# Optimization experiments

Measured on AMD Instinct MI355X. Metric: run time of the kernel, lower is better.

Reference implementation:

```python
import jax, jax.numpy as jnp
import numpy as np

EPS = 1e-5

def _bn(h, gamma, beta):
    # training-mode batch norm over dim 0 (biased variance, as torch)
    mu = h.mean(axis=0)
    var = ((h - mu) ** 2).mean(axis=0)
    return (h - mu) * jax.lax.rsqrt(var + EPS) * gamma + beta

def _mlp(h, W1, b1, g1, be1, W2, b2):
    # PyG MLP, num_layers=2: Linear -> BatchNorm -> ReLU -> Linear (dropout=0)
    h = h @ W1 + b1
    h = jax.nn.relu(_bn(h, g1, be1))
    return h @ W2 + b2

def setup_inputs() -> dict:
    key = jax.random.key(0)
    ks = jax.random.split(key, 12)
    N, E = 50000, 800000
    node_dim, edge_dim, hidden = 64, 64, 128
    d_in1 = node_dim + edge_dim   # 128
    d_in2 = node_dim + hidden     # 192
    def lin(k, fi, fo):
        s = 1.0 / np.sqrt(fi)
        return jax.random.uniform(k, (fi, fo), jnp.float32, -s, s)
    inp = {
        "x": jax.random.normal(ks[0], (N, node_dim), jnp.float32),
        "edge_index": jax.random.randint(ks[1], (2, E), 0, N, jnp.int32),
        "edge_attr": jax.random.normal(ks[2], (E, edge_dim), jnp.float32),
        "u": jax.random.normal(ks[3], (1, 16), jnp.float32),
        "batch": jnp.zeros((N,), jnp.int32),
        # node_mlp_1 params
        "W1a": lin(ks[4], d_in1, hidden), "b1a": jnp.zeros((hidden,), jnp.float32),
        "g1a": jnp.ones((hidden,), jnp.float32), "be1a": jnp.zeros((hidden,), jnp.float32),
        "W2a": lin(ks[5], hidden, hidden), "b2a": jnp.zeros((hidden,), jnp.float32),
        # node_mlp_2 params
        "W1b": lin(ks[6], d_in2, hidden), "b1b": jnp.zeros((hidden,), jnp.float32),
        "g1b": jnp.ones((hidden,), jnp.float32), "be1b": jnp.zeros((hidden,), jnp.float32),
        "W2b": lin(ks[7], hidden, node_dim), "b2b": jnp.zeros((node_dim,), jnp.float32),
    }
    return inp

def reference(x, edge_index, edge_attr, u, batch,
              W1a, b1a, g1a, be1a, W2a, b2a,
              W1b, b1b, g1b, be1b, W2b, b2b):
    row, col = edge_index[0], edge_index[1]
    # gather source nodes, concat edge features  -> [E, node_dim+edge_dim]
    out = jnp.concatenate([x[row], edge_attr], axis=1)
    out = _mlp(out, W1a, b1a, g1a, be1a, W2a, b2a)          # [E, hidden]
    out = jax.ops.segment_sum(out, col, num_segments=x.shape[0])  # scatter_add -> [N, hidden]
    out = jnp.concatenate([x, out], axis=1)                  # [N, node_dim+hidden]
    return _mlp(out, W1b, b1b, g1b, be1b, W2b, b2b)          # [N, node_dim]
```

## Files before the change

kernel.cpp:

```cpp
#include <hip/hip_runtime.h>
#include <hip/hip_fp16.h>


typedef _Float16 half8  __attribute__((ext_vector_type(8)));
typedef _Float16 half4h __attribute__((ext_vector_type(4)));
typedef float    floatx4 __attribute__((ext_vector_type(4)));

#define MFMA16(a, b, c) __builtin_amdgcn_mfma_f32_16x16x32_f16(a, b, c, 0, 0, 0)

#define LDS_BARRIER() do { \
    asm volatile("s_waitcnt lgkmcnt(0)" ::: "memory"); \
    __builtin_amdgcn_s_barrier(); \
} while (0)

__device__ __forceinline__ float col_reduce16(float v) {
    v += __shfl_xor(v, 16, 64);
    v += __shfl_xor(v, 32, 64);
    return v;
}

__global__ void k_prep(const float* __restrict__ w1a, const float* __restrict__ w2a,
                       const float* __restrict__ w1b, const float* __restrict__ w2b,
                       _Float16* __restrict__ w1at, _Float16* __restrict__ w2at,
                       _Float16* __restrict__ w1bt, _Float16* __restrict__ w2bt) {
    int i = blockIdx.x * 256 + threadIdx.x;
    if (i < 16384) {
        int n = i >> 7, k = i & 127;
        w1at[n * 128 + k] = (_Float16)w1a[k * 128 + n];
    } else if (i < 32768) {
        int j = i - 16384; int n = j >> 7, k = j & 127;
        w2at[n * 128 + k] = (_Float16)w2a[k * 128 + n];
    } else if (i < 57344) {
        int j = i - 32768; int n = j / 192, k = j - n * 192;
        w1bt[n * 192 + k] = (_Float16)w1b[k * 128 + n];
    } else if (i < 65536) {
        int j = i - 57344; int n = j >> 7, k = j & 127;
        w2bt[n * 128 + k] = (_Float16)w2b[k * 64 + n];
    }
}

__global__ __launch_bounds__(512, 4) void k_edge_stats(
    const float* __restrict__ x, const int* __restrict__ rowi,
    const float* __restrict__ ea, const _Float16* __restrict__ w1t,
    float* __restrict__ gsum, float* __restrict__ gsq, int nTiles) {
    __shared__ _Float16 sW[128][136];
    __shared__ _Float16 sIn[128][136];
    const int tid = threadIdx.x, lane = tid & 63, wv = tid >> 6;
    const int lm = lane & 15, q = lane >> 4, koff = q * 8;
    const int G = gridDim.x;
    const int e = tid >> 2, part = tid & 3;

    {
        int n = tid >> 2, seg = (tid & 3) * 32;
        const half8* src = (const half8*)(w1t + n * 128 + seg);
        half8* dst = (half8*)&sW[n][seg];
        dst[0] = src[0]; dst[1] = src[1]; dst[2] = src[2]; dst[3] = src[3];
    }
    float sAcc[8], ssAcc[8];
#pragma unroll
    for (int i = 0; i < 8; i++) { sAcc[i] = 0.f; ssAcc[i] = 0.f; }

    int t = blockIdx.x;
    floatx4 pv[8];
    {
        long ge = (long)t * 128 + e;
        const float* src = (part < 2) ? x + (long)rowi[ge] * 64 + part * 32
                                      : ea + ge * 64 + (part - 2) * 32;
#pragma unroll
        for (int i = 0; i < 8; i++) pv[i] = ((const floatx4*)src)[i];
    }
    for (; t < nTiles; t += G) {
        {
            _Float16* dst = &sIn[e][part * 32];
#pragma unroll
            for (int i = 0; i < 8; i++) {
                half4h h = {(_Float16)pv[i][0], (_Float16)pv[i][1],
                            (_Float16)pv[i][2], (_Float16)pv[i][3]};
                *(half4h*)(dst + i * 4) = h;
            }
        }
        LDS_BARRIER();
        int tn = t + G;
        if (tn < nTiles) {
            long ge = (long)tn * 128 + e;
            const float* src = (part < 2) ? x + (long)rowi[ge] * 64 + part * 32
                                          : ea + ge * 64 + (part - 2) * 32;
#pragma unroll
            for (int i = 0; i < 8; i++) pv[i] = ((const floatx4*)src)[i];
        }
        half8 a[4];
#pragma unroll
        for (int kb = 0; kb < 4; kb++)
            a[kb] = *(const half8*)&sIn[wv * 16 + lm][kb * 32 + koff];
#pragma unroll
        for (int nt = 0; nt < 8; nt++) {
            floatx4 acc = {0.f, 0.f, 0.f, 0.f};
            const int c = nt * 16 + lm;
#pragma unroll
            for (int kb = 0; kb < 4; kb++) {
                half8 b = *(const half8*)&sW[c][kb * 32 + koff];
                acc = MFMA16(a[kb], b, acc);
            }
            sAcc[nt]  += acc[0] + acc[1] + acc[2] + acc[3];
            ssAcc[nt] += acc[0]*acc[0] + acc[1]*acc[1] + acc[2]*acc[2] + acc[3]*acc[3];
        }
        LDS_BARRIER();
    }
#pragma unroll
    for (int nt = 0; nt < 8; nt++) {
        float s  = col_reduce16(sAcc[nt]);
        float ss = col_reduce16(ssAcc[nt]);
        if (q == 0) {
            int c = nt * 16 + lm;
            int slot = (blockIdx.x * 8 + wv) & 15;
            unsafeAtomicAdd(&gsum[slot * 128 + c], s);
            unsafeAtomicAdd(&gsq[slot * 128 + c], ss);
        }
    }
}

__global__ void k_finalize(const float* __restrict__ sums, const float* __restrict__ sqs,
                           const float* __restrict__ gamma, const float* __restrict__ beta,
                           float* __restrict__ scale, float* __restrict__ shift, float count) {
    int i = threadIdx.x;
    float s = 0.f, ssq = 0.f;
    for (int j = 0; j < 16; j++) { s += sums[j * 128 + i]; ssq += sqs[j * 128 + i]; }
    float mu = s / count;
    float var = ssq / count - mu * mu;
    float sc = gamma[i] * rsqrtf(var + 1e-5f);
    scale[i] = sc;
    shift[i] = beta[i] - mu * sc;
}

__global__ __launch_bounds__(512, 2) void k_edge_mlp(
    const float* __restrict__ x, const int* __restrict__ rowi, const int* __restrict__ coli,
    const float* __restrict__ ea, const _Float16* __restrict__ w1t, const _Float16* __restrict__ w2t,
    const float* __restrict__ scale, const float* __restrict__ shift, const float* __restrict__ b2a,
    __half* __restrict__ agg, int nTiles) {
    __shared__ _Float16 sW1[128][136];
    __shared__ _Float16 sW2[128][136];
    __shared__ _Float16 sIn[2][128][136];
    __shared__ float sScale[128], sShift[128], sB2[128];
    __shared__ int sCol[2][128];
    const int tid = threadIdx.x, lane = tid & 63, wv = tid >> 6;
    const int lm = lane & 15, q = lane >> 4, koff = q * 8;
    const int G = gridDim.x;
    const int e = tid >> 2, part = tid & 3;

    {
        int n = tid >> 2, seg = (tid & 3) * 32;
        const half8* s1 = (const half8*)(w1t + n * 128 + seg);
        half8* d1 = (half8*)&sW1[n][seg];
        d1[0] = s1[0]; d1[1] = s1[1]; d1[2] = s1[2]; d1[3] = s1[3];
        const half8* s2 = (const half8*)(w2t + n * 128 + seg);
        half8* d2 = (half8*)&sW2[n][seg];
        d2[0] = s2[0]; d2[1] = s2[1]; d2[2] = s2[2]; d2[3] = s2[3];
    }
    if (tid < 128) { sScale[tid] = scale[tid]; sShift[tid] = shift[tid]; sB2[tid] = b2a[tid]; }

    int t = blockIdx.x;
    {
        long ge = (long)t * 128 + e;
        const float* src = (part < 2) ? x + (long)rowi[ge] * 64 + part * 32
                                      : ea + ge * 64 + (part - 2) * 32;
        _Float16* dst = &sIn[0][e][part * 32];
#pragma unroll
        for (int i = 0; i < 8; i++) {
            floatx4 v = ((const floatx4*)src)[i];
            half4h h = {(_Float16)v[0], (_Float16)v[1], (_Float16)v[2], (_Float16)v[3]};
            *(half4h*)(dst + i * 4) = h;
        }
        if (tid < 128) sCol[0][tid] = coli[(long)t * 128 + tid];
    }
    __syncthreads();
    int p = 0;
    for (; t < nTiles; t += G) {
        half8 a[4];
#pragma unroll
        for (int kb = 0; kb < 4; kb++)
            a[kb] = *(const half8*)&sIn[p][wv * 16 + lm][kb * 32 + koff];
        int myCol[4];
#pragma unroll
        for (int r = 0; r < 4; r++) myCol[r] = sCol[p][wv * 16 + q * 4 + r];

        int tn = t + G; bool hasNext = tn < nTiles;
        floatx4 pv[8]; int pcol = 0;
        if (hasNext) {
            long ge = (long)tn * 128 + e;
            const float* src = (part < 2) ? x + (long)rowi[ge] * 64 + part * 32
                                          : ea + ge * 64 + (part - 2) * 32;
#pragma unroll
            for (int i = 0; i < 8; i++) pv[i] = ((const floatx4*)src)[i];
            if (tid < 128) pcol = coli[(long)tn * 128 + tid];
        }
        floatx4 acc1[8];
#pragma unroll
        for (int nt = 0; nt < 8; nt++) {
            floatx4 acc = {0.f, 0.f, 0.f, 0.f};
            const int c = nt * 16 + lm;
#pragma unroll
            for (int kb = 0; kb < 4; kb++) {
                half8 b = *(const half8*)&sW1[c][kb * 32 + koff];
                acc = MFMA16(a[kb], b, acc);
            }
            acc1[nt] = acc;
        }
        LDS_BARRIER();

        _Float16(*sT)[136] = sIn[p];
#pragma unroll
        for (int nt = 0; nt < 8; nt++) {
            const int c = nt * 16 + lm;
            float sc = sScale[c], sh = sShift[c];
            half4h h;
#pragma unroll
            for (int r = 0; r < 4; r++)
                h[r] = (_Float16)fmaxf(acc1[nt][r] * sc + sh, 0.f);
            *(half4h*)&sT[c][wv * 16 + q * 4] = h;
        }
        half8 a2[4];
#pragma unroll
        for (int kb = 0; kb < 4; kb++) {
#pragma unroll
            for (int j = 0; j < 8; j++)
                a2[kb][j] = sT[kb * 32 + koff + j][wv * 16 + lm];
        }
#pragma unroll
        for (int nt = 0; nt < 8; nt++) {
            floatx4 acc = {0.f, 0.f, 0.f, 0.f};
            const int c = nt * 16 + lm;
#pragma unroll
            for (int kb = 0; kb < 4; kb++) {
                half8 b = *(const half8*)&sW2[c][kb * 32 + koff];
                acc = MFMA16(a2[kb], b, acc);
            }
            acc1[nt] = acc;
        }
        if (hasNext) {
            _Float16* dst = &sIn[p ^ 1][e][part * 32];
#pragma unroll
            for (int i = 0; i < 8; i++) {
                half4h h = {(_Float16)pv[i][0], (_Float16)pv[i][1],
                            (_Float16)pv[i][2], (_Float16)pv[i][3]};
                *(half4h*)(dst + i * 4) = h;
            }
            if (tid < 128) sCol[p ^ 1][tid] = pcol;
        }
#pragma unroll
        for (int nt = 0; nt < 8; nt++) {
            const int c = nt * 16 + lm;
            const int c0 = c & ~1;
            float bb = sB2[c];
            float v0 = acc1[nt][0] + bb, v1 = acc1[nt][1] + bb;
            float v2 = acc1[nt][2] + bb, v3 = acc1[nt][3] + bb;
            float p0 = __shfl_xor(v0, 1, 64), p1 = __shfl_xor(v1, 1, 64);
            float p2 = __shfl_xor(v2, 1, 64), p3 = __shfl_xor(v3, 1, 64);
            if ((lane & 1) == 0) {
                unsafeAtomicAdd((__half2*)&agg[(size_t)myCol[0] * 128 + c0], __floats2half2_rn(v0, p0));
                unsafeAtomicAdd((__half2*)&agg[(size_t)myCol[1] * 128 + c0], __floats2half2_rn(v1, p1));
            } else {
                unsafeAtomicAdd((__half2*)&agg[(size_t)myCol[2] * 128 + c0], __floats2half2_rn(p2, v2));
                unsafeAtomicAdd((__half2*)&agg[(size_t)myCol[3] * 128 + c0], __floats2half2_rn(p3, v3));
            }
        }
        LDS_BARRIER();
        p ^= 1;
    }
}

__global__ __launch_bounds__(512, 2) void k_node_a(
    const float* __restrict__ x, const __half* __restrict__ agg,
    const _Float16* __restrict__ w1bt, float* __restrict__ h3,
    float* __restrict__ gsum, float* __restrict__ gsq, int N) {
    __shared__ _Float16 sIn[128][200];
    __shared__ _Float16 sW[128][200];
    __shared__ float sSum[128], sSq[128];
    const int tid = threadIdx.x, lane = tid & 63, wv = tid >> 6;
    const long e0 = (long)blockIdx.x * 128;

    {
        int n = tid >> 2, seg = (tid & 3) * 48;
        const half8* src = (const half8*)(w1bt + n * 192 + seg);
        half8* dst = (half8*)&sW[n][seg];
        dst[0] = src[0]; dst[1] = src[1]; dst[2] = src[2];
        dst[3] = src[3]; dst[4] = src[4]; dst[5] = src[5];
    }
    if (tid < 128) { sSum[tid] = 0.f; sSq[tid] = 0.f; }
    {
        int m = tid >> 2, seg = tid & 3;
        long gm = e0 + m;
        bool valid = gm < N;
        const float* srcx = x + gm * 64 + seg * 16;
        _Float16* dstx = &sIn[m][seg * 16];
#pragma unroll
        for (int i = 0; i < 4; i++) {
            floatx4 v = {0.f, 0.f, 0.f, 0.f};
            if (valid) v = ((const floatx4*)srcx)[i];
            half4h h = {(_Float16)v[0], (_Float16)v[1], (_Float16)v[2], (_Float16)v[3]};
            *(half4h*)(dstx + i * 4) = h;
        }
        const _Float16* srca = (const _Float16*)agg + gm * 128 + seg * 32;
        _Float16* dsta = &sIn[m][64 + seg * 32];
#pragma unroll
        for (int i = 0; i < 4; i++) {
            half8 v = {0, 0, 0, 0, 0, 0, 0, 0};
            if (valid) v = ((const half8*)srca)[i];
            *(half8*)(dsta + i * 8) = v;
        }
    }
    __syncthreads();

    const int lm = lane & 15, q = lane >> 4, koff = q * 8;
    half8 a[6];
#pragma unroll
    for (int kb = 0; kb < 6; kb++)
        a[kb] = *(const half8*)&sIn[wv * 16 + lm][kb * 32 + koff];
#pragma unroll
    for (int nt = 0; nt < 8; nt++) {
        floatx4 acc = {0.f, 0.f, 0.f, 0.f};
        const int c = nt * 16 + lm;
#pragma unroll
        for (int kb = 0; kb < 6; kb++) {
            half8 b = *(const half8*)&sW[c][kb * 32 + koff];
            acc = MFMA16(a[kb], b, acc);
        }
        float s  = acc[0] + acc[1] + acc[2] + acc[3];
        float ss = acc[0]*acc[0] + acc[1]*acc[1] + acc[2]*acc[2] + acc[3]*acc[3];
        s = col_reduce16(s); ss = col_reduce16(ss);
        if (q == 0) { atomicAdd(&sSum[c], s); atomicAdd(&sSq[c], ss); }
#pragma unroll
        for (int r = 0; r < 4; r++) {
            int m2 = wv * 16 + q * 4 + r;
            long gm2 = e0 + m2;
            if (gm2 < N) h3[gm2 * 128 + c] = acc[r];
        }
    }
    __syncthreads();
    if (tid < 128) {
        int slot = blockIdx.x & 15;
        unsafeAtomicAdd(&gsum[slot * 128 + tid], sSum[tid]);
        unsafeAtomicAdd(&gsq[slot * 128 + tid], sSq[tid]);
    }
}

__global__ __launch_bounds__(512, 2) void k_node_b(
    const float* __restrict__ h3, const _Float16* __restrict__ w2bt,
    const float* __restrict__ scale, const float* __restrict__ shift,
    const float* __restrict__ b2b, float* __restrict__ out, int N) {
    __shared__ _Float16 sH[128][136];
    __shared__ _Float16 sW[64][136];
    const int tid = threadIdx.x, lane = tid & 63, wv = tid >> 6;
    const long e0 = (long)blockIdx.x * 128;

    {
        int n = tid >> 3, seg = (tid & 7) * 16;
        const half8* src = (const half8*)(w2bt + n * 128 + seg);
        half8* dst = (half8*)&sW[n][seg];
        dst[0] = src[0]; dst[1] = src[1];
    }
    {
        int m = tid >> 2, seg = (tid & 3) * 32;
        long gm = e0 + m;
        bool valid = gm < N;
        const float* src = h3 + gm * 128 + seg;
        _Float16* dst = &sH[m][seg];
#pragma unroll
        for (int i = 0; i < 8; i++) {
            floatx4 v = {0.f, 0.f, 0.f, 0.f};
            if (valid) v = ((const floatx4*)src)[i];
            floatx4 sc = ((const floatx4*)(scale + seg))[i];
            floatx4 sh = ((const floatx4*)(shift + seg))[i];
            half4h h;
#pragma unroll
            for (int j = 0; j < 4; j++)
                h[j] = (_Float16)fmaxf(v[j] * sc[j] + sh[j], 0.f);
            *(half4h*)(dst + i * 4) = h;
        }
    }
    __syncthreads();

    const int lm = lane & 15, q = lane >> 4, koff = q * 8;
    half8 a[4];
#pragma unroll
    for (int kb = 0; kb < 4; kb++)
        a[kb] = *(const half8*)&sH[wv * 16 + lm][kb * 32 + koff];
#pragma unroll
    for (int nt = 0; nt < 4; nt++) {
        floatx4 acc = {0.f, 0.f, 0.f, 0.f};
        const int c = nt * 16 + lm;
#pragma unroll
        for (int kb = 0; kb < 4; kb++) {
            half8 b = *(const half8*)&sW[c][kb * 32 + koff];
            acc = MFMA16(a[kb], b, acc);
        }
        float bb = b2b[c];
#pragma unroll
        for (int r = 0; r < 4; r++) {
            int m2 = wv * 16 + q * 4 + r;
            long gm2 = e0 + m2;
            if (gm2 < N) out[gm2 * 64 + c] = acc[r] + bb;
        }
    }
}

extern "C" void kernel_launch(void* const* d_in, const int* in_sizes, int n_in,
                              void* d_out, int out_size, void* d_ws, size_t ws_size,
                              hipStream_t stream) {
    const float* x    = (const float*)d_in[0];
    const int*   eidx = (const int*)d_in[1];
    const float* ea   = (const float*)d_in[2];
    const float* W1a  = (const float*)d_in[5];
    const float* g1a  = (const float*)d_in[7];
    const float* be1a = (const float*)d_in[8];
    const float* W2a  = (const float*)d_in[9];
    const float* b2a  = (const float*)d_in[10];
    const float* W1b  = (const float*)d_in[11];
    const float* g1b  = (const float*)d_in[13];
    const float* be1b = (const float*)d_in[14];
    const float* W2b  = (const float*)d_in[15];
    const float* b2b  = (const float*)d_in[16];
    const int N = in_sizes[0] / 64;
    const int E = in_sizes[2] / 64;
    const int* rowi = eidx;
    const int* coli = eidx + E;

    float* ws   = (float*)d_ws;
    __half* agg = (__half*)ws;
    float* h3   = ws + (size_t)N * 64;
    float* st   = h3 + (size_t)N * 128;
    float* sumE = st,        * sqE = st + 2048;
    float* sumN = st + 4096, * sqN = st + 6144;
    float* scE  = st + 8192, * shE = st + 8320;
    float* scN  = st + 8448, * shN = st + 8576;
    _Float16* wh   = (_Float16*)(st + 8704);
    _Float16* w1at = wh;
    _Float16* w2at = wh + 16384;
    _Float16* w1bt = wh + 32768;
    _Float16* w2bt = wh + 57344;

    hipMemsetAsync(agg, 0, (size_t)N * 128 * sizeof(__half), stream);
    hipMemsetAsync(st, 0, 8192 * sizeof(float), stream);
    k_prep<<<256, 256, 0, stream>>>(W1a, W2a, W1b, W2b, w1at, w2at, w1bt, w2bt);

    int nTilesE = E / 128;
    int nbl = (N + 127) / 128;
    k_edge_stats<<<500, 512, 0, stream>>>(x, rowi, ea, w1at, sumE, sqE, nTilesE);
    k_finalize<<<1, 128, 0, stream>>>(sumE, sqE, g1a, be1a, scE, shE, (float)E);
    k_edge_mlp<<<250, 512, 0, stream>>>(x, rowi, coli, ea, w1at, w2at, scE, shE, b2a, agg, nTilesE);
    k_node_a<<<nbl, 512, 0, stream>>>(x, agg, w1bt, h3, sumN, sqN, N);
    k_finalize<<<1, 128, 0, stream>>>(sumN, sqN, g1b, be1b, scN, shN, (float)N);
    k_node_b<<<nbl, 512, 0, stream>>>(h3, w2bt, scN, shN, b2b, (float*)d_out, N);
}
```

Measured before the change: 723.0 us.

## Sort edges by destination and segment-reduce within tiles before atomic adds

Adds a counting sort of edges by destination node (histogram, single-block scan, atomic scatter) that builds permuted row, edge-id and column arrays. The edge MLP kernel then reads edges in destination order and performs a segmented reduction across the 16-row MFMA tile using shuffles, so only one atomic add per run of equal destinations is issued. This is meant to cut the half2 atomic traffic into the aggregation buffer. In exchange it adds three preprocessing kernels, a serial-ish 1024-thread scan, and random (non-coalesced) reads of edge_attr via edge ids.

```diff
diff --git a/kernel.cpp b/kernel.cpp
--- a/kernel.cpp
+++ b/kernel.cpp
@@ -39,6 +39,49 @@
     }
 }
 
+__global__ void k_hist(const int* __restrict__ coli, int* __restrict__ cnt, int E) {
+    int i = blockIdx.x * 512 + threadIdx.x;
+    if (i < E) atomicAdd(&cnt[coli[i]], 1);
+}
+
+__global__ __launch_bounds__(1024) void k_scan(const int* __restrict__ cnt,
+                                               int* __restrict__ cur, int N) {
+    __shared__ int sp[1024];
+    int t = threadIdx.x;
+    int chunk = (N + 1023) >> 10;
+    int base = t * chunk;
+    int s = 0;
+    for (int j = 0; j < chunk; j++) {
+        int idx = base + j;
+        if (idx < N) s += cnt[idx];
+    }
+    sp[t] = s; __syncthreads();
+    for (int off = 1; off < 1024; off <<= 1) {
+        int v = (t >= off) ? sp[t - off] : 0;
+        __syncthreads();
+        sp[t] += v;
+        __syncthreads();
+    }
+    int run = sp[t] - s;
+    for (int j = 0; j < chunk; j++) {
+        int idx = base + j;
+        if (idx < N) { cur[idx] = run; run += cnt[idx]; }
+    }
+}
+
+__global__ void k_scatter(const int* __restrict__ rowi, const int* __restrict__ coli,
+                          int* __restrict__ cur, int* __restrict__ rowp,
+                          int* __restrict__ eidp, int* __restrict__ colp, int E) {
+    int i = blockIdx.x * 512 + threadIdx.x;
+    if (i < E) {
+        int c = coli[i];
+        int p = atomicAdd(&cur[c], 1);
+        rowp[p] = rowi[i];
+        eidp[p] = i;
+        colp[p] = c;
+    }
+}
+
 __global__ __launch_bounds__(512, 4) void k_edge_stats(
     const float* __restrict__ x, const int* __restrict__ rowi,
     const float* __restrict__ ea, const _Float16* __restrict__ w1t,
@@ -133,7 +176,8 @@
 }
 
 __global__ __launch_bounds__(512, 2) void k_edge_mlp(
-    const float* __restrict__ x, const int* __restrict__ rowi, const int* __restrict__ coli,
+    const float* __restrict__ x, const int* __restrict__ rowp, const int* __restrict__ eidp,
+    const int* __restrict__ colp,
     const float* __restrict__ ea, const _Float16* __restrict__ w1t, const _Float16* __restrict__ w2t,
     const float* __restrict__ scale, const float* __restrict__ shift, const float* __restrict__ b2a,
     __half* __restrict__ agg, int nTiles) {
@@ -161,8 +205,9 @@
     int t = blockIdx.x;
     {
         long ge = (long)t * 128 + e;
-        const float* src = (part < 2) ? x + (long)rowi[ge] * 64 + part * 32
-                                      : ea + ge * 64 + (part - 2) * 32;
+        int idx = (part < 2) ? rowp[ge] : eidp[ge];
+        const float* src = (part < 2) ? x + (long)idx * 64 + part * 32
+                                      : ea + (long)idx * 64 + (part - 2) * 32;
         _Float16* dst = &sIn[0][e][part * 32];
 #pragma unroll
         for (int i = 0; i < 8; i++) {
@@ -170,7 +215,7 @@
             half4h h = {(_Float16)v[0], (_Float16)v[1], (_Float16)v[2], (_Float16)v[3]};
             *(half4h*)(dst + i * 4) = h;
         }
-        if (tid < 128) sCol[0][tid] = coli[(long)t * 128 + tid];
+        if (tid < 128) sCol[0][tid] = colp[(long)t * 128 + tid];
     }
     __syncthreads();
     int p = 0;
@@ -180,18 +225,35 @@
         for (int kb = 0; kb < 4; kb++)
             a[kb] = *(const half8*)&sIn[p][wv * 16 + lm][kb * 32 + koff];
         int myCol[4];
-#pragma unroll
-        for (int r = 0; r < 4; r++) myCol[r] = sCol[p][wv * 16 + q * 4 + r];
+        const int m0 = wv * 16 + q * 4;
+#pragma unroll
+        for (int r = 0; r < 4; r++) myCol[r] = sCol[p][m0 + r];
+        int cp = sCol[p][(q > 0) ? m0 - 1 : m0];
+        int cn = sCol[p][(q < 3) ? m0 + 4 : m0 + 3];
+        const bool h0 = (q == 0) || (myCol[0] != cp);
+        const bool h1 = myCol[1] != myCol[0];
+        const bool h2 = myCol[2] != myCol[1];
+        const bool h3 = myCol[3] != myCol[2];
+        const bool t0 = h1, t1 = h2, t2 = h3;
+        const bool t3 = (q == 3) || (myCol[3] != cn);
+        const bool c0m = !h0, c1m = c0m && !h1, c2m = c1m && !h2, c3m = c2m && !h3;
+        const int F0 = (h0 | h1 | h2 | h3) ? 1 : 0;
+        int Fp1 = __shfl(F0, (lane - 16) & 63, 64);
+        const bool add1 = (q >= 1) && !F0;
+        const int F1 = (F0 || ((q >= 1) && Fp1)) ? 1 : 0;
+        const bool add2 = (q >= 2) && !F1;
+        const bool useC = (q >= 1) && !h0;
 
         int tn = t + G; bool hasNext = tn < nTiles;
         floatx4 pv[8]; int pcol = 0;
         if (hasNext) {
             long ge = (long)tn * 128 + e;
-            const float* src = (part < 2) ? x + (long)rowi[ge] * 64 + part * 32
-                                          : ea + ge * 64 + (part - 2) * 32;
+            int idx = (part < 2) ? rowp[ge] : eidp[ge];
+            const float* src = (part < 2) ? x + (long)idx * 64 + part * 32
+                                          : ea + (long)idx * 64 + (part - 2) * 32;
 #pragma unroll
             for (int i = 0; i < 8; i++) pv[i] = ((const floatx4*)src)[i];
-            if (tid < 128) pcol = coli[(long)tn * 128 + tid];
+            if (tid < 128) pcol = colp[(long)tn * 128 + tid];
         }
         floatx4 acc1[8];
 #pragma unroll
@@ -253,14 +315,29 @@
             float bb = sB2[c];
             float v0 = acc1[nt][0] + bb, v1 = acc1[nt][1] + bb;
             float v2 = acc1[nt][2] + bb, v3 = acc1[nt][3] + bb;
-            float p0 = __shfl_xor(v0, 1, 64), p1 = __shfl_xor(v1, 1, 64);
-            float p2 = __shfl_xor(v2, 1, 64), p3 = __shfl_xor(v3, 1, 64);
+            float s0 = v0;
+            float s1 = h1 ? v1 : (s0 + v1);
+            float s2 = h2 ? v2 : (s1 + v2);
+            float s3 = h3 ? v3 : (s2 + v3);
+            float S = s3;
+            float Sp = __shfl(S, (lane - 16) & 63, 64);
+            if (add1) S += Sp;
+            float Sq = __shfl(S, (lane - 32) & 63, 64);
+            if (add2) S += Sq;
+            float Cc = __shfl(S, (lane - 16) & 63, 64);
+            float C = useC ? Cc : 0.f;
+            float f0 = c0m ? (s0 + C) : s0;
+            float f1 = c1m ? (s1 + C) : s1;
+            float f2 = c2m ? (s2 + C) : s2;
+            float f3 = c3m ? (s3 + C) : s3;
+            float g0 = __shfl_xor(f0, 1, 64), g1 = __shfl_xor(f1, 1, 64);
+            float g2 = __shfl_xor(f2, 1, 64), g3 = __shfl_xor(f3, 1, 64);
             if ((lane & 1) == 0) {
-                unsafeAtomicAdd((__half2*)&agg[(size_t)myCol[0] * 128 + c0], __floats2half2_rn(v0, p0));
-                unsafeAtomicAdd((__half2*)&agg[(size_t)myCol[1] * 128 + c0], __floats2half2_rn(v1, p1));
+                if (t0) unsafeAtomicAdd((__half2*)&agg[(size_t)myCol[0] * 128 + c0], __floats2half2_rn(f0, g0));
+                if (t1) unsafeAtomicAdd((__half2*)&agg[(size_t)myCol[1] * 128 + c0], __floats2half2_rn(f1, g1));
             } else {
-                unsafeAtomicAdd((__half2*)&agg[(size_t)myCol[2] * 128 + c0], __floats2half2_rn(p2, v2));
-                unsafeAtomicAdd((__half2*)&agg[(size_t)myCol[3] * 128 + c0], __floats2half2_rn(p3, v3));
+                if (t2) unsafeAtomicAdd((__half2*)&agg[(size_t)myCol[2] * 128 + c0], __floats2half2_rn(g2, f2));
+                if (t3) unsafeAtomicAdd((__half2*)&agg[(size_t)myCol[3] * 128 + c0], __floats2half2_rn(g3, f3));
             }
         }
         LDS_BARRIER();
@@ -437,16 +514,27 @@
     _Float16* w2at = wh + 16384;
     _Float16* w1bt = wh + 32768;
     _Float16* w2bt = wh + 57344;
+    int* cnt  = (int*)(wh + 65536);
+    int* cur  = cnt + N;
+    int* rowp = cur + N;
+    int* eidp = rowp + E;
+    int* colp = eidp + E;
 
     hipMemsetAsync(agg, 0, (size_t)N * 128 * sizeof(__half), stream);
     hipMemsetAsync(st, 0, 8192 * sizeof(float), stream);
+    hipMemsetAsync(cnt, 0, (size_t)N * sizeof(int), stream);
     k_prep<<<256, 256, 0, stream>>>(W1a, W2a, W1b, W2b, w1at, w2at, w1bt, w2bt);
+
+    int nbE = (E + 511) / 512;
+    k_hist<<<nbE, 512, 0, stream>>>(coli, cnt, E);
+    k_scan<<<1, 1024, 0, stream>>>(cnt, cur, N);
+    k_scatter<<<nbE, 512, 0, stream>>>(rowi, coli, cur, rowp, eidp, colp, E);
 
     int nTilesE = E / 128;
     int nbl = (N + 127) / 128;
     k_edge_stats<<<500, 512, 0, stream>>>(x, rowi, ea, w1at, sumE, sqE, nTilesE);
     k_finalize<<<1, 128, 0, stream>>>(sumE, sqE, g1a, be1a, scE, shE, (float)E);
-    k_edge_mlp<<<250, 512, 0, stream>>>(x, rowi, coli, ea, w1at, w2at, scE, shE, b2a, agg, nTilesE);
+    k_edge_mlp<<<250, 512, 0, stream>>>(x, rowp, eidp, colp, ea, w1at, w2at, scE, shE, b2a, agg, nTilesE);
     k_node_a<<<nbl, 512, 0, stream>>>(x, agg, w1bt, h3, sumN, sqN, N);
     k_finalize<<<1, 128, 0, stream>>>(sumN, sqN, g1b, be1b, scN, shN, (float)N);
     k_node_b<<<nbl, 512, 0, stream>>>(h3, w2bt, scN, shN, b2b, (float*)d_out, N);
```

After: 742.3 us. 1.03x slower.
